# Kernel tuning notes

Measured on AMD Instinct MI355X. Metric: run time of the kernel, lower is better.

Reference implementation:

```python
import jax, jax.numpy as jnp
import numpy as np

B, T, F_IN, H = 512, 512, 64, 128
BN_EPS = 1e-3  # Keras BatchNormalization default epsilon


def setup_inputs() -> dict:
    key = jax.random.key(0)
    ks = jax.random.split(key, 12)
    x = jax.random.normal(ks[0], (B, T, F_IN), dtype=jnp.float32)
    # last channel is a discrete phase index in {0,1,2}, stored as float
    state = jax.random.randint(ks[1], (B, T, 1), 0, 3).astype(jnp.float32)
    inputs = jnp.concatenate([x, state], axis=-1)  # [B, T, F_IN+1]
    s = 1.0 / np.sqrt(H)
    return {
        "inputs": inputs,
        "Wx": jax.random.normal(ks[2], (F_IN, 3 * H), dtype=jnp.float32) * s,
        "Wh": jax.random.normal(ks[3], (H, 3 * H), dtype=jnp.float32) * s,
        "b": jax.random.normal(ks[4], (2, 3 * H), dtype=jnp.float32) * 0.01,
        "W_state": jax.random.normal(ks[5], (3, H), dtype=jnp.float32),
        "w1": jax.random.normal(ks[6], (H, 64), dtype=jnp.float32) * s,
        "b1": jnp.zeros((64,), jnp.float32),
        "gamma": jnp.ones((64,), jnp.float32),
        "beta": jnp.zeros((64,), jnp.float32),
        "mean": jnp.zeros((64,), jnp.float32),
        "var": jnp.ones((64,), jnp.float32),
        "w2": jax.random.normal(ks[7], (64, 1), dtype=jnp.float32) * 0.125,
        "b2": jnp.zeros((1,), jnp.float32),
    }


def _gru_final_state(x, Wx, Wh, b):
    # Keras GRU, reset_after=True (default): separate input / recurrent biases.
    b_in, b_rec = b[0], b[1]
    xw = x @ Wx + b_in                      # [B, T, 3H] (precompute input matmuls)
    xw_t = jnp.swapaxes(xw, 0, 1)           # [T, B, 3H]
    h0 = jnp.zeros((x.shape[0], Wh.shape[0]), x.dtype)

    def step(h, xw_step):
        rec = h @ Wh + b_rec                # [B, 3H]
        xz, xr, xh = jnp.split(xw_step, 3, axis=-1)
        rz, rr, rh = jnp.split(rec, 3, axis=-1)
        z = jax.nn.sigmoid(xz + rz)
        r = jax.nn.sigmoid(xr + rr)
        hh = jnp.tanh(xh + r * rh)
        h_new = z * h + (1.0 - z) * hh
        return h_new, None

    h_final, _ = jax.lax.scan(step, h0, xw_t)
    return h_final                          # [B, H]


def reference(inputs, Wx, Wh, b, W_state, w1, b1, gamma, beta, mean, var, w2, b2):
    x = inputs[:, :, :-1]                   # [B, T, F_IN]
    state = inputs[:, :, -1]                # [B, T]
    hidden = _gru_final_state(x, Wx, Wh, b)  # [B, H]
    idx = jnp.clip(state[:, -1].astype(jnp.int32), 0, W_state.shape[0] - 1)
    hidden = hidden + W_state[idx]          # gather-add phase effect
    h = jax.nn.relu(hidden @ w1 + b1)       # dense1
    # dropout: identity in inference mode
    h = (h - mean) * jax.lax.rsqrt(var + BN_EPS) * gamma + beta  # batchnorm (inference)
    return h @ w2 + b2                      # [B, 1]
```

## Files before the change

kernel.cpp:

```cpp
#include <hip/hip_runtime.h>
#include <hip/hip_bf16.h>

#define T_SEQ   512
#define H_DIM   128
#define N3H     384
#define HS      136
#define XS      72

typedef float f32x4 __attribute__((ext_vector_type(4)));
typedef float f32x2 __attribute__((ext_vector_type(2)));
typedef float f32x4u __attribute__((ext_vector_type(4), aligned(4)));
typedef __bf16 bf16x8 __attribute__((ext_vector_type(8)));
typedef unsigned short us8 __attribute__((ext_vector_type(8)));
typedef unsigned short us4 __attribute__((ext_vector_type(4)));

static __device__ __forceinline__ unsigned short f2bf(float f) {
    unsigned int u = __builtin_bit_cast(unsigned int, f);
    u += 0x7FFFu + ((u >> 16) & 1u);
    return (unsigned short)(u >> 16);
}

static __device__ __forceinline__ void lds_barrier() {
    asm volatile("" ::: "memory");
    __builtin_amdgcn_s_waitcnt(0xC07F);
    __builtin_amdgcn_s_barrier();
    asm volatile("" ::: "memory");
}

static __device__ __forceinline__ bf16x8 ld8(const unsigned short* p) {
    return __builtin_bit_cast(bf16x8, *(const us8*)p);
}

__global__ __launch_bounds__(512, 1) void gru_fused(
    const float* __restrict__ inputs, const float* __restrict__ Wx,
    const float* __restrict__ Wh, const float* __restrict__ bias,
    const float* __restrict__ W_state, const float* __restrict__ w1,
    const float* __restrict__ b1, const float* __restrict__ gamma,
    const float* __restrict__ beta, const float* __restrict__ mean,
    const float* __restrict__ var, const float* __restrict__ w2,
    const float* __restrict__ b2, float* __restrict__ out)
{
    __shared__ __attribute__((aligned(16))) unsigned short hb[2][16 * HS];
    __shared__ __attribute__((aligned(16))) unsigned short xb[2][16 * XS];
    __shared__ float hf[16][H_DIM + 1];

    const int tid  = threadIdx.x;
    const int w    = tid >> 6;
    const int lane = tid & 63;
    const int m    = lane & 15;
    const int q    = lane >> 4;
    const int b0   = blockIdx.x * 16;

    bf16x8 whB[3][4];
    bf16x8 wxB[3][2];
    float brec[3], bin[3];
#pragma unroll
    for (int g = 0; g < 3; ++g) {
        const int col = (8 * g + w) * 16 + m;
#pragma unroll
        for (int k = 0; k < 4; ++k) {
            us8 tmp;
#pragma unroll
            for (int j = 0; j < 8; ++j) tmp[j] = f2bf(Wh[(32 * k + 8 * q + j) * N3H + col]);
            whB[g][k] = __builtin_bit_cast(bf16x8, tmp);
        }
#pragma unroll
        for (int k = 0; k < 2; ++k) {
            us8 tmp;
#pragma unroll
            for (int j = 0; j < 8; ++j) tmp[j] = f2bf(Wx[(32 * k + 8 * q + j) * N3H + col]);
            wxB[g][k] = __builtin_bit_cast(bf16x8, tmp);
        }
        bin[g]  = bias[col];
        brec[g] = bias[N3H + col];
    }

    int hro[4], xro[2];
#pragma unroll
    for (int k = 0; k < 4; ++k) hro[k] = m * HS + 32 * k + 8 * q;
#pragma unroll
    for (int k = 0; k < 2; ++k) xro[k] = m * XS + 32 * k + 8 * q;
    const int hw_base = (4 * q) * HS + 16 * w + m;

    const int sr = tid >> 4, sc = tid & 15;
    const int xwoff = sr * XS + sc * 4;
    const float* xsrc = inputs + ((size_t)(b0 + sr) * T_SEQ) * 65 + sc * 4;

    auto xpack = [&](f32x4u v) -> us4 {
        us4 r; r[0] = f2bf(v[0]); r[1] = f2bf(v[1]); r[2] = f2bf(v[2]); r[3] = f2bf(v[3]);
        return r;
    };

    {
        unsigned int* p = (unsigned int*)hb[0];
        for (int i = tid; i < 16 * HS / 2; i += 512) p[i] = 0;
    }
    if (tid < 256) {
        f32x4u v0 = *(const f32x4u*)(xsrc + 0 * 65);
        f32x4u v1 = *(const f32x4u*)(xsrc + 1 * 65);
        *(us4*)&xb[0][xwoff] = xpack(v0);
        *(us4*)&xb[1][xwoff] = xpack(v1);
    }
    lds_barrier();

    f32x4 xwA[3], xwB[3];
    {
        bf16x8 xa[2];
#pragma unroll
        for (int k = 0; k < 2; ++k) xa[k] = ld8(&xb[0][xro[k]]);
#pragma unroll
        for (int g = 0; g < 3; ++g) {
            f32x4 acc = { bin[g], bin[g], bin[g], bin[g] };
            acc = __builtin_amdgcn_mfma_f32_16x16x32_bf16(xa[0], wxB[g][0], acc, 0, 0, 0);
            acc = __builtin_amdgcn_mfma_f32_16x16x32_bf16(xa[1], wxB[g][1], acc, 0, 0, 0);
            xwA[g] = acc;
        }
    }

    f32x4u pf0 = {}, pf1 = {};
    if (tid < 256) pf0 = *(const f32x4u*)(xsrc + 2 * 65);

    f32x4 hreg = { 0.f, 0.f, 0.f, 0.f };

    const float K1 = -1.4426950408889634f;
    const float K2 = -2.8853900817779268f;

    auto step = [&](int t, f32x4* xw_cur, f32x4* xw_next,
                    f32x4u& pfLoad, f32x4u& pfUse,
                    const unsigned short* hcur, unsigned short* hnxt,
                    const unsigned short* xnxt, unsigned short* xwr) {
        if (tid < 256 && t <= T_SEQ - 4) pfLoad = *(const f32x4u*)(xsrc + (t + 3) * 65);

        lds_barrier();

        bf16x8 ha[4];
#pragma unroll
        for (int k = 0; k < 4; ++k) ha[k] = ld8(&hcur[hro[k]]);
        f32x4 racc[3];
#pragma unroll
        for (int g = 0; g < 3; ++g) {
            f32x4 a1 = { brec[g], brec[g], brec[g], brec[g] };
            a1 = __builtin_amdgcn_mfma_f32_16x16x32_bf16(ha[0], whB[g][0], a1, 0, 0, 0);
            a1 = __builtin_amdgcn_mfma_f32_16x16x32_bf16(ha[1], whB[g][1], a1, 0, 0, 0);
            f32x4 a2 = { 0.f, 0.f, 0.f, 0.f };
            a2 = __builtin_amdgcn_mfma_f32_16x16x32_bf16(ha[2], whB[g][2], a2, 0, 0, 0);
            a2 = __builtin_amdgcn_mfma_f32_16x16x32_bf16(ha[3], whB[g][3], a2, 0, 0, 0);
            racc[g] = a1 + a2;
        }

        if (t < T_SEQ - 1) {
            bf16x8 xa[2];
#pragma unroll
            for (int k = 0; k < 2; ++k) xa[k] = ld8(&xnxt[xro[k]]);
#pragma unroll
            for (int g = 0; g < 3; ++g) {
                f32x4 acc = { bin[g], bin[g], bin[g], bin[g] };
                acc = __builtin_amdgcn_mfma_f32_16x16x32_bf16(xa[0], wxB[g][0], acc, 0, 0, 0);
                acc = __builtin_amdgcn_mfma_f32_16x16x32_bf16(xa[1], wxB[g][1], acc, 0, 0, 0);
                xw_next[g] = acc;
            }
        }

        f32x4 hnew;
#pragma unroll
        for (int i = 0; i < 4; ++i) {
            const float az = K1 * (xw_cur[0][i] + racc[0][i]);
            const float ar = K1 * (xw_cur[1][i] + racc[1][i]);
            const float ea = __builtin_amdgcn_exp2f(az);
            const float eb = __builtin_amdgcn_exp2f(ar);
            const float Pa = 1.0f + ea, Pb = 1.0f + eb;
            const float D  = __builtin_amdgcn_rcpf(Pa * Pb);
            const float z  = Pb * D;
            const float r  = Pa * D;
            float u = xw_cur[2][i] + r * racc[2][i];
            u = fminf(fmaxf(u, -15.0f), 15.0f);
            const float ec = __builtin_amdgcn_exp2f(K2 * u);
            const float T  = (1.0f - ec) * __builtin_amdgcn_rcpf(1.0f + ec);
            hnew[i] = T + z * (hreg[i] - T);
        }
        hreg = hnew;

#pragma unroll
        for (int i = 0; i < 4; ++i) hnxt[hw_base + i * HS] = f2bf(hnew[i]);

        if (tid < 256 && t <= T_SEQ - 3) *(us4*)&xwr[xwoff] = xpack(pfUse);
    };

    for (int t = 0; t < T_SEQ; t += 2) {
        step(t,     xwA, xwB, pf1, pf0, hb[0], hb[1], xb[1], xb[0]);
        step(t + 1, xwB, xwA, pf0, pf1, hb[1], hb[0], xb[0], xb[1]);
    }

#pragma unroll
    for (int i = 0; i < 4; ++i)
        hf[4 * q + i][16 * w + m] = hreg[i];
    __syncthreads();

    {
        const int row = tid >> 5;
        const int c0  = (tid & 31) * 4;
        const float sf = inputs[((size_t)(b0 + row) * T_SEQ + (T_SEQ - 1)) * 65 + 64];
        int si = (int)sf;
        si = si < 0 ? 0 : (si > 2 ? 2 : si);
#pragma unroll
        for (int c = 0; c < 4; ++c)
            hf[row][c0 + c] += W_state[si * H_DIM + c0 + c];
    }
    __syncthreads();

    {
        const int row = tid >> 5;
        const int jj  = (tid & 31) * 2;
        f32x2 acc = { b1[jj], b1[jj + 1] };
        for (int k = 0; k < H_DIM; ++k) {
            const float hv = hf[row][k];
            const f32x2 wv = *(const f32x2*)(w1 + k * 64 + jj);
            acc[0] = fmaf(hv, wv[0], acc[0]);
            acc[1] = fmaf(hv, wv[1], acc[1]);
        }
        float v = 0.0f;
#pragma unroll
        for (int ii = 0; ii < 2; ++ii) {
            const int j = jj + ii;
            float a = fmaxf(acc[ii], 0.0f);
            a = (a - mean[j]) * rsqrtf(var[j] + 1e-3f) * gamma[j] + beta[j];
            v = fmaf(a, w2[j], v);
        }
        v += __shfl_down(v, 16);
        v += __shfl_down(v, 8);
        v += __shfl_down(v, 4);
        v += __shfl_down(v, 2);
        v += __shfl_down(v, 1);
        if ((tid & 31) == 0) out[b0 + row] = v + b2[0];
    }
}

extern "C" void kernel_launch(void* const* d_in, const int* in_sizes, int n_in,
                              void* d_out, int out_size, void* d_ws, size_t ws_size,
                              hipStream_t stream) {
    (void)in_sizes; (void)n_in; (void)out_size; (void)d_ws; (void)ws_size;
    const float* inputs  = (const float*)d_in[0];
    const float* Wx      = (const float*)d_in[1];
    const float* Wh      = (const float*)d_in[2];
    const float* bias    = (const float*)d_in[3];
    const float* W_state = (const float*)d_in[4];
    const float* w1      = (const float*)d_in[5];
    const float* b1      = (const float*)d_in[6];
    const float* gamma   = (const float*)d_in[7];
    const float* beta    = (const float*)d_in[8];
    const float* mean    = (const float*)d_in[9];
    const float* var     = (const float*)d_in[10];
    const float* w2      = (const float*)d_in[11];
    const float* b2      = (const float*)d_in[12];
    float* out = (float*)d_out;

    gru_fused<<<32, 512, 0, stream>>>(inputs, Wx, Wh, bias, W_state, w1, b1,
                                      gamma, beta, mean, var, w2, b2, out);
}
```

Before: 500.0 us.

## Precompute input projections in a parallel prepass and stream them into the recurrence

Adds a separate kernel that computes x@Wx+b_in for all timesteps across 1024 blocks and stores the result as bf16 in workspace. The recurrent kernel then loads the precomputed projections from global memory two steps ahead, instead of staging x through LDS and running the input MFMAs inside the serial loop. This shortens the per-step critical path of the 32-block recurrence. The cost is an extra launch, a roughly 100 MB intermediate buffer written and read back, and extra bf16 rounding of the projections. The old fused kernel is kept as a fallback when the workspace is too small.

```diff
diff --git a/kernel.cpp b/kernel.cpp
--- a/kernel.cpp
+++ b/kernel.cpp
@@ -19,6 +19,9 @@
     u += 0x7FFFu + ((u >> 16) & 1u);
     return (unsigned short)(u >> 16);
 }
+static __device__ __forceinline__ float bf2f(unsigned short u) {
+    return __builtin_bit_cast(float, ((unsigned int)u) << 16);
+}
 
 static __device__ __forceinline__ void lds_barrier() {
     asm volatile("" ::: "memory");
@@ -31,7 +34,213 @@
     return __builtin_bit_cast(bf16x8, *(const us8*)p);
 }
 
-__global__ __launch_bounds__(512, 1) void gru_fused(
+__global__ __launch_bounds__(512, 1) void xw_prepass(
+    const float* __restrict__ inputs, const float* __restrict__ Wx,
+    const float* __restrict__ bias, unsigned short* __restrict__ xwbuf)
+{
+    const int tid  = threadIdx.x;
+    const int w    = tid >> 6;
+    const int lane = tid & 63;
+    const int m    = lane & 15;
+    const int q    = lane >> 4;
+    const int bt   = blockIdx.x & 31;
+    const int tc   = blockIdx.x >> 5;
+    const int b0   = bt * 16;
+
+    bf16x8 wxB[3][2];
+    float bin[3];
+#pragma unroll
+    for (int g = 0; g < 3; ++g) {
+        const int col = (8 * g + w) * 16 + m;
+#pragma unroll
+        for (int k = 0; k < 2; ++k) {
+            us8 tmp;
+#pragma unroll
+            for (int j = 0; j < 8; ++j) tmp[j] = f2bf(Wx[(32 * k + 8 * q + j) * N3H + col]);
+            wxB[g][k] = __builtin_bit_cast(bf16x8, tmp);
+        }
+        bin[g] = bias[col];
+    }
+
+    const float* xr = inputs + ((size_t)(b0 + m) * T_SEQ + (size_t)tc * 16) * 65;
+
+    for (int tt = 0; tt < 16; ++tt) {
+        const int t = tc * 16 + tt;
+        bf16x8 xa[2];
+#pragma unroll
+        for (int k = 0; k < 2; ++k) {
+            f32x4u lo = *(const f32x4u*)(xr + (size_t)tt * 65 + 32 * k + 8 * q);
+            f32x4u hi = *(const f32x4u*)(xr + (size_t)tt * 65 + 32 * k + 8 * q + 4);
+            us8 tmp;
+#pragma unroll
+            for (int j = 0; j < 4; ++j) { tmp[j] = f2bf(lo[j]); tmp[4 + j] = f2bf(hi[j]); }
+            xa[k] = __builtin_bit_cast(bf16x8, tmp);
+        }
+#pragma unroll
+        for (int g = 0; g < 3; ++g) {
+            f32x4 acc = { bin[g], bin[g], bin[g], bin[g] };
+            acc = __builtin_amdgcn_mfma_f32_16x16x32_bf16(xa[0], wxB[g][0], acc, 0, 0, 0);
+            acc = __builtin_amdgcn_mfma_f32_16x16x32_bf16(xa[1], wxB[g][1], acc, 0, 0, 0);
+            us4 o; o[0] = f2bf(acc[0]); o[1] = f2bf(acc[1]); o[2] = f2bf(acc[2]); o[3] = f2bf(acc[3]);
+            *(us4*)(xwbuf + (((size_t)t * 32 + bt) * 24 + (8 * g + w)) * 256 + lane * 4) = o;
+        }
+    }
+}
+
+__global__ __launch_bounds__(512, 1) void gru_fused_pre(
+    const float* __restrict__ inputs, const float* __restrict__ Wh,
+    const float* __restrict__ bias, const unsigned short* __restrict__ xwbuf,
+    const float* __restrict__ W_state, const float* __restrict__ w1,
+    const float* __restrict__ b1, const float* __restrict__ gamma,
+    const float* __restrict__ beta, const float* __restrict__ mean,
+    const float* __restrict__ var, const float* __restrict__ w2,
+    const float* __restrict__ b2, float* __restrict__ out)
+{
+    __shared__ __attribute__((aligned(16))) unsigned short hb[2][16 * HS];
+    __shared__ float hf[16][H_DIM + 1];
+
+    const int tid  = threadIdx.x;
+    const int w    = tid >> 6;
+    const int lane = tid & 63;
+    const int m    = lane & 15;
+    const int q    = lane >> 4;
+    const int b0   = blockIdx.x * 16;
+
+    bf16x8 whB[3][4];
+    float brec[3];
+#pragma unroll
+    for (int g = 0; g < 3; ++g) {
+        const int col = (8 * g + w) * 16 + m;
+#pragma unroll
+        for (int k = 0; k < 4; ++k) {
+            us8 tmp;
+#pragma unroll
+            for (int j = 0; j < 8; ++j) tmp[j] = f2bf(Wh[(32 * k + 8 * q + j) * N3H + col]);
+            whB[g][k] = __builtin_bit_cast(bf16x8, tmp);
+        }
+        brec[g] = bias[N3H + col];
+    }
+
+    int hro[4];
+#pragma unroll
+    for (int k = 0; k < 4; ++k) hro[k] = m * HS + 32 * k + 8 * q;
+    const int hw_base = (4 * q) * HS + 16 * w + m;
+
+    const us4* xwb[3];
+#pragma unroll
+    for (int g = 0; g < 3; ++g)
+        xwb[g] = (const us4*)xwbuf + ((size_t)blockIdx.x * 24 + (8 * g + w)) * 64 + lane;
+    const size_t TSTRIDE = (size_t)32 * 24 * 64;
+
+    {
+        unsigned int* p = (unsigned int*)hb[0];
+        for (int i = tid; i < 16 * HS / 2; i += 512) p[i] = 0;
+    }
+
+    us4 slot[2][3];
+#pragma unroll
+    for (int g = 0; g < 3; ++g) {
+        slot[0][g] = xwb[g][0];
+        slot[1][g] = xwb[g][TSTRIDE];
+    }
+
+    f32x4 hreg = { 0.f, 0.f, 0.f, 0.f };
+    const float K1 = -1.4426950408889634f;
+    const float K2 = -2.8853900817779268f;
+
+    auto step = [&](int t, int p, const unsigned short* hcur, unsigned short* hnxt) {
+        f32x4 xwf[3];
+#pragma unroll
+        for (int g = 0; g < 3; ++g)
+#pragma unroll
+            for (int i = 0; i < 4; ++i) xwf[g][i] = bf2f(slot[p][g][i]);
+        if (t + 2 < T_SEQ) {
+#pragma unroll
+            for (int g = 0; g < 3; ++g) slot[p][g] = xwb[g][(size_t)(t + 2) * TSTRIDE];
+        }
+
+        lds_barrier();
+
+        bf16x8 ha[4];
+#pragma unroll
+        for (int k = 0; k < 4; ++k) ha[k] = ld8(&hcur[hro[k]]);
+        f32x4 racc[3];
+#pragma unroll
+        for (int g = 0; g < 3; ++g) {
+            f32x4 a1 = { brec[g], brec[g], brec[g], brec[g] };
+            a1 = __builtin_amdgcn_mfma_f32_16x16x32_bf16(ha[0], whB[g][0], a1, 0, 0, 0);
+            a1 = __builtin_amdgcn_mfma_f32_16x16x32_bf16(ha[1], whB[g][1], a1, 0, 0, 0);
+            f32x4 a2 = { 0.f, 0.f, 0.f, 0.f };
+            a2 = __builtin_amdgcn_mfma_f32_16x16x32_bf16(ha[2], whB[g][2], a2, 0, 0, 0);
+            a2 = __builtin_amdgcn_mfma_f32_16x16x32_bf16(ha[3], whB[g][3], a2, 0, 0, 0);
+            racc[g] = a1 + a2;
+        }
+
+        f32x4 hnew;
+#pragma unroll
+        for (int i = 0; i < 4; ++i) {
+            const float ea = __builtin_amdgcn_exp2f(K1 * (xwf[0][i] + racc[0][i]));
+            const float eb = __builtin_amdgcn_exp2f(K1 * (xwf[1][i] + racc[1][i]));
+            const float Pa = 1.0f + ea, Pb = 1.0f + eb;
+            const float D  = __builtin_amdgcn_rcpf(Pa * Pb);
+            const float z  = Pb * D;
+            const float r  = Pa * D;
+            float u = __builtin_amdgcn_fmed3f(xwf[2][i] + r * racc[2][i], -15.0f, 15.0f);
+            const float ec = __builtin_amdgcn_exp2f(K2 * u);
+            const float T  = (1.0f - ec) * __builtin_amdgcn_rcpf(1.0f + ec);
+            hnew[i] = T + z * (hreg[i] - T);
+        }
+        hreg = hnew;
+#pragma unroll
+        for (int i = 0; i < 4; ++i) hnxt[hw_base + i * HS] = f2bf(hnew[i]);
+    };
+
+    for (int t = 0; t < T_SEQ; t += 2) {
+        step(t,     0, hb[0], hb[1]);
+        step(t + 1, 1, hb[1], hb[0]);
+    }
+
+#pragma unroll
+    for (int i = 0; i < 4; ++i) hf[4 * q + i][16 * w + m] = hreg[i];
+    __syncthreads();
+    {
+        const int row = tid >> 5;
+        const int c0  = (tid & 31) * 4;
+        const float sf = inputs[((size_t)(b0 + row) * T_SEQ + (T_SEQ - 1)) * 65 + 64];
+        int si = (int)sf;
+        si = si < 0 ? 0 : (si > 2 ? 2 : si);
+#pragma unroll
+        for (int c = 0; c < 4; ++c) hf[row][c0 + c] += W_state[si * H_DIM + c0 + c];
+    }
+    __syncthreads();
+    {
+        const int row = tid >> 5;
+        const int jj  = (tid & 31) * 2;
+        f32x2 acc = { b1[jj], b1[jj + 1] };
+        for (int k = 0; k < H_DIM; ++k) {
+            const float hv = hf[row][k];
+            const f32x2 wv = *(const f32x2*)(w1 + k * 64 + jj);
+            acc[0] = fmaf(hv, wv[0], acc[0]);
+            acc[1] = fmaf(hv, wv[1], acc[1]);
+        }
+        float v = 0.0f;
+#pragma unroll
+        for (int ii = 0; ii < 2; ++ii) {
+            const int j = jj + ii;
+            float a = fmaxf(acc[ii], 0.0f);
+            a = (a - mean[j]) * rsqrtf(var[j] + 1e-3f) * gamma[j] + beta[j];
+            v = fmaf(a, w2[j], v);
+        }
+        v += __shfl_down(v, 16);
+        v += __shfl_down(v, 8);
+        v += __shfl_down(v, 4);
+        v += __shfl_down(v, 2);
+        v += __shfl_down(v, 1);
+        if ((tid & 31) == 0) out[b0 + row] = v + b2[0];
+    }
+}
+
+__global__ __launch_bounds__(512, 1) void gru_fused_fb(
     const float* __restrict__ inputs, const float* __restrict__ Wx,
     const float* __restrict__ Wh, const float* __restrict__ bias,
     const float* __restrict__ W_state, const float* __restrict__ w1,
@@ -121,7 +330,6 @@
     if (tid < 256) pf0 = *(const f32x4u*)(xsrc + 2 * 65);
 
     f32x4 hreg = { 0.f, 0.f, 0.f, 0.f };
-
     const float K1 = -1.4426950408889634f;
     const float K2 = -2.8853900817779268f;
 
@@ -130,9 +338,7 @@
                     const unsigned short* hcur, unsigned short* hnxt,
                     const unsigned short* xnxt, unsigned short* xwr) {
         if (tid < 256 && t <= T_SEQ - 4) pfLoad = *(const f32x4u*)(xsrc + (t + 3) * 65);
-
         lds_barrier();
-
         bf16x8 ha[4];
 #pragma unroll
         for (int k = 0; k < 4; ++k) ha[k] = ld8(&hcur[hro[k]]);
@@ -147,7 +353,6 @@
             a2 = __builtin_amdgcn_mfma_f32_16x16x32_bf16(ha[3], whB[g][3], a2, 0, 0, 0);
             racc[g] = a1 + a2;
         }
-
         if (t < T_SEQ - 1) {
             bf16x8 xa[2];
 #pragma unroll
@@ -160,29 +365,23 @@
                 xw_next[g] = acc;
             }
         }
-
         f32x4 hnew;
 #pragma unroll
         for (int i = 0; i < 4; ++i) {
-            const float az = K1 * (xw_cur[0][i] + racc[0][i]);
-            const float ar = K1 * (xw_cur[1][i] + racc[1][i]);
-            const float ea = __builtin_amdgcn_exp2f(az);
-            const float eb = __builtin_amdgcn_exp2f(ar);
+            const float ea = __builtin_amdgcn_exp2f(K1 * (xw_cur[0][i] + racc[0][i]));
+            const float eb = __builtin_amdgcn_exp2f(K1 * (xw_cur[1][i] + racc[1][i]));
             const float Pa = 1.0f + ea, Pb = 1.0f + eb;
             const float D  = __builtin_amdgcn_rcpf(Pa * Pb);
             const float z  = Pb * D;
             const float r  = Pa * D;
-            float u = xw_cur[2][i] + r * racc[2][i];
-            u = fminf(fmaxf(u, -15.0f), 15.0f);
+            float u = __builtin_amdgcn_fmed3f(xw_cur[2][i] + r * racc[2][i], -15.0f, 15.0f);
             const float ec = __builtin_amdgcn_exp2f(K2 * u);
             const float T  = (1.0f - ec) * __builtin_amdgcn_rcpf(1.0f + ec);
             hnew[i] = T + z * (hreg[i] - T);
         }
         hreg = hnew;
-
 #pragma unroll
         for (int i = 0; i < 4; ++i) hnxt[hw_base + i * HS] = f2bf(hnew[i]);
-
         if (tid < 256 && t <= T_SEQ - 3) *(us4*)&xwr[xwoff] = xpack(pfUse);
     };
 
@@ -192,10 +391,8 @@
     }
 
 #pragma unroll
-    for (int i = 0; i < 4; ++i)
-        hf[4 * q + i][16 * w + m] = hreg[i];
+    for (int i = 0; i < 4; ++i) hf[4 * q + i][16 * w + m] = hreg[i];
     __syncthreads();
-
     {
         const int row = tid >> 5;
         const int c0  = (tid & 31) * 4;
@@ -203,11 +400,9 @@
         int si = (int)sf;
         si = si < 0 ? 0 : (si > 2 ? 2 : si);
 #pragma unroll
-        for (int c = 0; c < 4; ++c)
-            hf[row][c0 + c] += W_state[si * H_DIM + c0 + c];
+        for (int c = 0; c < 4; ++c) hf[row][c0 + c] += W_state[si * H_DIM + c0 + c];
     }
     __syncthreads();
-
     {
         const int row = tid >> 5;
         const int jj  = (tid & 31) * 2;
@@ -238,7 +433,7 @@
 extern "C" void kernel_launch(void* const* d_in, const int* in_sizes, int n_in,
                               void* d_out, int out_size, void* d_ws, size_t ws_size,
                               hipStream_t stream) {
-    (void)in_sizes; (void)n_in; (void)out_size; (void)d_ws; (void)ws_size;
+    (void)in_sizes; (void)n_in; (void)out_size;
     const float* inputs  = (const float*)d_in[0];
     const float* Wx      = (const float*)d_in[1];
     const float* Wh      = (const float*)d_in[2];
@@ -254,6 +449,16 @@
     const float* b2      = (const float*)d_in[12];
     float* out = (float*)d_out;
 
-    gru_fused<<<32, 512, 0, stream>>>(inputs, Wx, Wh, bias, W_state, w1, b1,
-                                      gamma, beta, mean, var, w2, b2, out);
-}
+    const size_t xw_bytes = (size_t)T_SEQ * 32 * 24 * 256 * sizeof(unsigned short);
+    if (ws_size >= xw_bytes) {
+        unsigned short* xwbuf = (unsigned short*)d_ws;
+        xw_prepass<<<1024, 512, 0, stream>>>(inputs, Wx, bias, xwbuf);
+        gru_fused_pre<<<32, 512, 0, stream>>>(inputs, Wh, bias, xwbuf, W_state,
+                                              w1, b1, gamma, beta, mean, var,
+                                              w2, b2, out);
+    } else {
+        gru_fused_fb<<<32, 512, 0, stream>>>(inputs, Wx, Wh, bias, W_state, w1,
+                                             b1, gamma, beta, mean, var, w2, b2,
+                                             out);
+    }
+}
```

New measurement: 565.4 us. 1.13x slower.

## Fold activation scales into GRU weights, swizzle hidden LDS layout, reorder step

Applied to the files above, without the earlier changes.

Pre-scales the z/r gate weights and biases by -log2(e) and the candidate gate by 2*log2(e) when converting to bf16. This removes per-element multiplies and the tanh clamp from the serial recurrence, and tanh is rewritten as 1-2/(1+e). The hidden-state LDS buffer drops its padding in favour of an XOR swizzle for bank-conflict avoidance. The next step's input MFMAs are moved after the gate math so the h update and store come sooner on the critical path. Scaling before bf16 rounding changes rounding slightly, and removing the clamp relies on exp2 overflow giving the correct saturated tanh limits.

```diff
diff --git a/kernel.cpp b/kernel.cpp
--- a/kernel.cpp
+++ b/kernel.cpp
@@ -4,7 +4,7 @@
 #define T_SEQ   512
 #define H_DIM   128
 #define N3H     384
-#define HS      136
+#define HSW     128
 #define XS      72
 
 typedef float f32x4 __attribute__((ext_vector_type(4)));
@@ -40,7 +40,7 @@
     const float* __restrict__ var, const float* __restrict__ w2,
     const float* __restrict__ b2, float* __restrict__ out)
 {
-    __shared__ __attribute__((aligned(16))) unsigned short hb[2][16 * HS];
+    __shared__ __attribute__((aligned(16))) unsigned short hb[2][16 * HSW];
     __shared__ __attribute__((aligned(16))) unsigned short xb[2][16 * XS];
     __shared__ float hf[16][H_DIM + 1];
 
@@ -51,36 +51,44 @@
     const int q    = lane >> 4;
     const int b0   = blockIdx.x * 16;
 
+    const float SCL0 = -1.4426950408889634f;
+    const float SCL2 =  2.8853900817779268f;
+
     bf16x8 whB[3][4];
     bf16x8 wxB[3][2];
     float brec[3], bin[3];
 #pragma unroll
     for (int g = 0; g < 3; ++g) {
+        const float s = (g < 2) ? SCL0 : SCL2;
         const int col = (8 * g + w) * 16 + m;
 #pragma unroll
         for (int k = 0; k < 4; ++k) {
             us8 tmp;
 #pragma unroll
-            for (int j = 0; j < 8; ++j) tmp[j] = f2bf(Wh[(32 * k + 8 * q + j) * N3H + col]);
+            for (int j = 0; j < 8; ++j) tmp[j] = f2bf(s * Wh[(32 * k + 8 * q + j) * N3H + col]);
             whB[g][k] = __builtin_bit_cast(bf16x8, tmp);
         }
 #pragma unroll
         for (int k = 0; k < 2; ++k) {
             us8 tmp;
 #pragma unroll
-            for (int j = 0; j < 8; ++j) tmp[j] = f2bf(Wx[(32 * k + 8 * q + j) * N3H + col]);
+            for (int j = 0; j < 8; ++j) tmp[j] = f2bf(s * Wx[(32 * k + 8 * q + j) * N3H + col]);
             wxB[g][k] = __builtin_bit_cast(bf16x8, tmp);
         }
-        bin[g]  = bias[col];
-        brec[g] = bias[N3H + col];
-    }
-
-    int hro[4], xro[2];
-#pragma unroll
-    for (int k = 0; k < 4; ++k) hro[k] = m * HS + 32 * k + 8 * q;
+        bin[g]  = s * bias[col];
+        brec[g] = s * bias[N3H + col];
+    }
+
+    int hro[4], hwo[4], xro[2];
+#pragma unroll
+    for (int k = 0; k < 4; ++k) hro[k] = m * HSW + (((4 * k + q) ^ (m & 7)) * 8);
+#pragma unroll
+    for (int i = 0; i < 4; ++i) {
+        const int row = 4 * q + i;
+        hwo[i] = row * HSW + (((2 * w + (m >> 3)) ^ (row & 7)) * 8) + (m & 7);
+    }
 #pragma unroll
     for (int k = 0; k < 2; ++k) xro[k] = m * XS + 32 * k + 8 * q;
-    const int hw_base = (4 * q) * HS + 16 * w + m;
 
     const int sr = tid >> 4, sc = tid & 15;
     const int xwoff = sr * XS + sc * 4;
@@ -93,7 +101,7 @@
 
     {
         unsigned int* p = (unsigned int*)hb[0];
-        for (int i = tid; i < 16 * HS / 2; i += 512) p[i] = 0;
+        for (int i = tid; i < 16 * HSW / 2; i += 512) p[i] = 0;
     }
     if (tid < 256) {
         f32x4u v0 = *(const f32x4u*)(xsrc + 0 * 65);
@@ -122,9 +130,6 @@
 
     f32x4 hreg = { 0.f, 0.f, 0.f, 0.f };
 
-    const float K1 = -1.4426950408889634f;
-    const float K2 = -2.8853900817779268f;
-
     auto step = [&](int t, f32x4* xw_cur, f32x4* xw_next,
                     f32x4u& pfLoad, f32x4u& pfUse,
                     const unsigned short* hcur, unsigned short* hnxt,
@@ -136,6 +141,12 @@
         bf16x8 ha[4];
 #pragma unroll
         for (int k = 0; k < 4; ++k) ha[k] = ld8(&hcur[hro[k]]);
+        bf16x8 xa[2];
+        if (t < T_SEQ - 1) {
+#pragma unroll
+            for (int k = 0; k < 2; ++k) xa[k] = ld8(&xnxt[xro[k]]);
+        }
+
         f32x4 racc[3];
 #pragma unroll
         for (int g = 0; g < 3; ++g) {
@@ -148,10 +159,23 @@
             racc[g] = a1 + a2;
         }
 
+        f32x4 hnew;
+#pragma unroll
+        for (int i = 0; i < 4; ++i) {
+            const float ea = __builtin_amdgcn_exp2f(xw_cur[0][i] + racc[0][i]);
+            const float eb = __builtin_amdgcn_exp2f(xw_cur[1][i] + racc[1][i]);
+            const float Pa = 1.0f + ea, Pb = 1.0f + eb;
+            const float D  = __builtin_amdgcn_rcpf(Pa * Pb);
+            const float z  = Pb * D;
+            const float r  = Pa * D;
+            const float u  = fmaf(r, racc[2][i], xw_cur[2][i]);
+            const float ec = __builtin_amdgcn_exp2f(u);
+            const float hh = fmaf(-2.0f, __builtin_amdgcn_rcpf(1.0f + ec), 1.0f);
+            hnew[i] = fmaf(z, hreg[i] - hh, hh);
+        }
+        hreg = hnew;
+
         if (t < T_SEQ - 1) {
-            bf16x8 xa[2];
-#pragma unroll
-            for (int k = 0; k < 2; ++k) xa[k] = ld8(&xnxt[xro[k]]);
 #pragma unroll
             for (int g = 0; g < 3; ++g) {
                 f32x4 acc = { bin[g], bin[g], bin[g], bin[g] };
@@ -161,27 +185,8 @@
             }
         }
 
-        f32x4 hnew;
-#pragma unroll
-        for (int i = 0; i < 4; ++i) {
-            const float az = K1 * (xw_cur[0][i] + racc[0][i]);
-            const float ar = K1 * (xw_cur[1][i] + racc[1][i]);
-            const float ea = __builtin_amdgcn_exp2f(az);
-            const float eb = __builtin_amdgcn_exp2f(ar);
-            const float Pa = 1.0f + ea, Pb = 1.0f + eb;
-            const float D  = __builtin_amdgcn_rcpf(Pa * Pb);
-            const float z  = Pb * D;
-            const float r  = Pa * D;
-            float u = xw_cur[2][i] + r * racc[2][i];
-            u = fminf(fmaxf(u, -15.0f), 15.0f);
-            const float ec = __builtin_amdgcn_exp2f(K2 * u);
-            const float T  = (1.0f - ec) * __builtin_amdgcn_rcpf(1.0f + ec);
-            hnew[i] = T + z * (hreg[i] - T);
-        }
-        hreg = hnew;
-
-#pragma unroll
-        for (int i = 0; i < 4; ++i) hnxt[hw_base + i * HS] = f2bf(hnew[i]);
+#pragma unroll
+        for (int i = 0; i < 4; ++i) hnxt[hwo[i]] = f2bf(hnew[i]);
 
         if (tid < 256 && t <= T_SEQ - 3) *(us4*)&xwr[xwoff] = xpack(pfUse);
     };
```

Measured after the change: 475.9 us. 4.8% less time.
